# Optimization experiments

Measured on AMD Instinct MI355X. Metric: run time of the kernel, lower is better.

## Reference

```python
import jax, jax.numpy as jnp
import numpy as np

B, L, D, H = 2, 2048, 1024, 16
DK = D // H
DFF = 4 * D
EPS = 1e-5  # torch LayerNorm default


def setup_inputs() -> dict:
    key = jax.random.key(0)
    ks = jax.random.split(key, 12)
    w = lambda k, shp: (jax.random.normal(k, shp, jnp.float32) * 0.02)
    return {
        "x": jax.random.normal(ks[0], (B, L, D), jnp.float32),
        "y": jax.random.normal(ks[1], (B, L, D), jnp.float32),
        "Wq": w(ks[2], (D, D)), "bq": jnp.zeros((D,), jnp.float32),
        "Wk": w(ks[3], (D, D)), "bk": jnp.zeros((D,), jnp.float32),
        "Wv": w(ks[4], (D, D)), "bv": jnp.zeros((D,), jnp.float32),
        "Wo": w(ks[5], (D, D)), "bo": jnp.zeros((D,), jnp.float32),
        "W1": w(ks[6], (D, DFF)), "b1": jnp.zeros((DFF,), jnp.float32),
        "W2": w(ks[7], (DFF, D)), "b2": jnp.zeros((D,), jnp.float32),
        "ln1_w": jnp.ones((L, D), jnp.float32), "ln1_b": jnp.zeros((L, D), jnp.float32),
        "ln2_w": jnp.ones((L, D), jnp.float32), "ln2_b": jnp.zeros((L, D), jnp.float32),
    }


def _layernorm2d(t, w, b):
    # nn.LayerNorm(normalized_shape=[L, D]): normalize jointly over last two dims
    mu = jnp.mean(t, axis=(-2, -1), keepdims=True)
    var = jnp.mean((t - mu) ** 2, axis=(-2, -1), keepdims=True)
    return (t - mu) * jax.lax.rsqrt(var + EPS) * w + b


def _attention(q_in, kv_in, Wq, bq, Wk, bk, Wv, bv, Wo, bo):
    split = lambda t: t.reshape(B, L, H, DK).transpose(0, 2, 1, 3)  # [B,H,L,DK]
    q = split(q_in @ Wq + bq)
    k = split(kv_in @ Wk + bk)
    v = split(kv_in @ Wv + bv)
    scores = jnp.einsum("bhqd,bhkd->bhqk", q, k) / (DK ** 0.5)
    # NOTE: original applies torch.tril to SCORES (zeroes upper triangle,
    # NOT -inf), so future positions still contribute exp(0)=1 in softmax.
    scores = jnp.tril(scores)
    p_attn = jax.nn.softmax(scores, axis=-1)
    out = jnp.einsum("bhqk,bhkd->bhqd", p_attn, v)
    out = out.transpose(0, 2, 1, 3).reshape(B, L, D)
    return out @ Wo + bo


def reference(x, y, Wq, bq, Wk, bk, Wv, bv, Wo, bo, W1, b1, W2, b2,
              ln1_w, ln1_b, ln2_w, ln2_b):
    # sublayer 0: pre-norm y, attention(query=x, key=value=norm(y)), residual
    y1 = y + _attention(x, _layernorm2d(y, ln1_w, ln1_b),
                        Wq, bq, Wk, bk, Wv, bv, Wo, bo)
    # sublayer 1: pre-norm, FFN (dropout inactive in eval), residual
    h = jax.nn.relu(_layernorm2d(y1, ln2_w, ln2_b) @ W1 + b1)
    return y1 + h @ W2 + b2
```

## Files before the change

kernel.cpp:

```cpp
#include <hip/hip_runtime.h>
#include <math.h>

#define B 2
#define L 2048
#define D 1024
#define H 16
#define DK 64
#define DFF 4096
#define EPS 1e-5f

typedef short short8 __attribute__((ext_vector_type(8)));
typedef short short4v __attribute__((ext_vector_type(4)));
typedef float float4v __attribute__((ext_vector_type(4)));
typedef unsigned int u32;

__device__ inline short f2bf(float f) {
    unsigned u = __builtin_bit_cast(unsigned, f);
    u += 0x7fffu + ((u >> 16) & 1u);
    return (short)(u >> 16);
}

__device__ inline float bf2f(short s) {
    unsigned u = ((unsigned)(unsigned short)s) << 16;
    return __builtin_bit_cast(float, u);
}

#define GLOAD_LDS16(gp, lp)                                                  \
    __builtin_amdgcn_global_load_lds(                                        \
        (const __attribute__((address_space(1))) u32*)(const void*)(gp),     \
        (__attribute__((address_space(3))) u32*)(void*)(lp), 16, 0, 0)


__global__ __launch_bounds__(256) void red_partial(const float* __restrict__ X,
                                                   float* __restrict__ part) {
    int b = blockIdx.y;
    const float4* p = (const float4*)(X + (size_t)b * L * D);
    float s = 0.f, ss = 0.f;
    for (int idx = blockIdx.x * 256 + threadIdx.x; idx < L * D / 4; idx += 256 * 256) {
        float4 v = p[idx];
        s += v.x + v.y + v.z + v.w;
        ss += v.x * v.x + v.y * v.y + v.z * v.z + v.w * v.w;
    }
    __shared__ float sh0[256], sh1[256];
    sh0[threadIdx.x] = s; sh1[threadIdx.x] = ss;
    __syncthreads();
    for (int o = 128; o; o >>= 1) {
        if (threadIdx.x < o) {
            sh0[threadIdx.x] += sh0[threadIdx.x + o];
            sh1[threadIdx.x] += sh1[threadIdx.x + o];
        }
        __syncthreads();
    }
    if (threadIdx.x == 0) {
        part[(b * 256 + blockIdx.x) * 2 + 0] = sh0[0];
        part[(b * 256 + blockIdx.x) * 2 + 1] = sh1[0];
    }
}

__global__ __launch_bounds__(256) void red_final(const float* __restrict__ part,
                                                 float* __restrict__ stats) {
    int b = blockIdx.x;
    float s = part[(b * 256 + threadIdx.x) * 2 + 0];
    float ss = part[(b * 256 + threadIdx.x) * 2 + 1];
    __shared__ float sh0[256], sh1[256];
    sh0[threadIdx.x] = s; sh1[threadIdx.x] = ss;
    __syncthreads();
    for (int o = 128; o; o >>= 1) {
        if (threadIdx.x < o) {
            sh0[threadIdx.x] += sh0[threadIdx.x + o];
            sh1[threadIdx.x] += sh1[threadIdx.x + o];
        }
        __syncthreads();
    }
    if (threadIdx.x == 0) {
        const float invN = 1.f / (float)(L * D);
        float mu = sh0[0] * invN;
        float var = sh1[0] * invN - mu * mu;
        stats[b * 2 + 0] = mu;
        stats[b * 2 + 1] = rsqrtf(var + EPS);
    }
}

__global__ __launch_bounds__(256) void ln_apply_bf(const float* __restrict__ X,
                                                   const float* __restrict__ W,
                                                   const float* __restrict__ Bb,
                                                   const float* __restrict__ stats,
                                                   short* __restrict__ Yn) {
    int b = blockIdx.y;
    float mu = stats[b * 2 + 0];
    float rstd = stats[b * 2 + 1];
    size_t e = (size_t)(blockIdx.x * 256 + threadIdx.x) * 4;
    const float4 xv = *(const float4*)(X + (size_t)b * L * D + e);
    const float4 wv = *(const float4*)(W + e);
    const float4 bv = *(const float4*)(Bb + e);
    short4v o;
    o[0] = f2bf((xv.x - mu) * rstd * wv.x + bv.x);
    o[1] = f2bf((xv.y - mu) * rstd * wv.y + bv.y);
    o[2] = f2bf((xv.z - mu) * rstd * wv.z + bv.z);
    o[3] = f2bf((xv.w - mu) * rstd * wv.w + bv.w);
    *(short4v*)(Yn + (size_t)b * L * D + e) = o;
}

__global__ __launch_bounds__(256) void convert_bf(const float* __restrict__ X,
                                                  short* __restrict__ Y) {
    size_t e = (size_t)(blockIdx.x * 256 + threadIdx.x) * 4;
    const float4 v = *(const float4*)(X + e);
    short4v o = {f2bf(v.x), f2bf(v.y), f2bf(v.z), f2bf(v.w)};
    *(short4v*)(Y + e) = o;
}

__global__ __launch_bounds__(256) void wt_transpose(const float* __restrict__ W,
                                                    short* __restrict__ WT,
                                                    int K, int N) {
    __shared__ short tile[32][33];
    const int t = threadIdx.x;
    const int tx = t & 31, ty = t >> 5;
    const int k0 = blockIdx.y * 32, n0 = blockIdx.x * 32;
#pragma unroll
    for (int i = 0; i < 4; ++i) {
        const int k = ty + i * 8;
        tile[k][tx] = f2bf(W[(size_t)(k0 + k) * N + n0 + tx]);
    }
    __syncthreads();
#pragma unroll
    for (int i = 0; i < 4; ++i) {
        const int n = ty + i * 8;
        WT[(size_t)(n0 + n) * K + k0 + tx] = tile[tx][n];
    }
}


__global__ __launch_bounds__(256) void gemm_mfma(const short* __restrict__ A,
                                                 const short* __restrict__ BT,
                                                 const float* __restrict__ bias,
                                                 const float* __restrict__ Res,
                                                 void* __restrict__ Cout,
                                                 int M, int N, int K, int flags) {
    __shared__ short As[128 * 32];
    __shared__ short Bs[128 * 32];
    const int t = threadIdx.x;
    const int wave = t >> 6, lane = t & 63;
    const int m16 = lane & 15, q4 = lane >> 4;
    const int m0 = blockIdx.y * 128, n0 = blockIdx.x * 128;
    const int wm = (wave >> 1) * 64, wn = (wave & 1) * 64;

    float4v acc[4][4];
#pragma unroll
    for (int i = 0; i < 4; ++i)
#pragma unroll
        for (int j = 0; j < 4; ++j) acc[i][j] = (float4v){0.f, 0.f, 0.f, 0.f};

    for (int k0 = 0; k0 < K; k0 += 32) {
        __syncthreads();
#pragma unroll
        for (int pass = 0; pass < 2; ++pass) {
            const int idx = pass * 256 + t;
            const int row = idx >> 2;
            const int ko = (idx & 3) * 8;
            short* ldsA = &As[(pass * 256 + wave * 64) * 8];
            short* ldsB = &Bs[(pass * 256 + wave * 64) * 8];
            GLOAD_LDS16(A + (size_t)(m0 + row) * K + k0 + ko, ldsA);
            GLOAD_LDS16(BT + (size_t)(n0 + row) * K + k0 + ko, ldsB);
        }
        __syncthreads();

        short8 af[4], bf[4];
#pragma unroll
        for (int mi = 0; mi < 4; ++mi)
            af[mi] = *(const short8*)&As[(wm + mi * 16 + m16) * 32 + q4 * 8];
#pragma unroll
        for (int ni = 0; ni < 4; ++ni)
            bf[ni] = *(const short8*)&Bs[(wn + ni * 16 + m16) * 32 + q4 * 8];
#pragma unroll
        for (int mi = 0; mi < 4; ++mi)
#pragma unroll
            for (int ni = 0; ni < 4; ++ni)
                acc[mi][ni] = __builtin_amdgcn_mfma_f32_16x16x32_bf16(
                    af[mi], bf[ni], acc[mi][ni], 0, 0, 0);
    }

#pragma unroll
    for (int mi = 0; mi < 4; ++mi)
#pragma unroll
        for (int ni = 0; ni < 4; ++ni) {
            const int col = n0 + wn + ni * 16 + m16;
            const float bb = bias[col];
#pragma unroll
            for (int r = 0; r < 4; ++r) {
                const int row = m0 + wm + mi * 16 + q4 * 4 + r;
                float v = acc[mi][ni][r] + bb;
                if (Res) v += Res[(size_t)row * N + col];
                if (flags & 1) v = fmaxf(v, 0.f);
                if (flags & 2)
                    ((short*)Cout)[(size_t)row * N + col] = f2bf(v);
                else
                    ((float*)Cout)[(size_t)row * N + col] = v;
            }
        }
}


__global__ __launch_bounds__(256) void gemm_mfma_64(const short* __restrict__ A,
                                                    const short* __restrict__ BT,
                                                    const float* __restrict__ bias,
                                                    const float* __restrict__ Res,
                                                    void* __restrict__ Cout,
                                                    int M, int N, int K, int flags) {
    __shared__ short As[64 * 32];
    __shared__ short Bs[128 * 32];
    const int t = threadIdx.x;
    const int wave = t >> 6, lane = t & 63;
    const int m16 = lane & 15, q4 = lane >> 4;
    const int m0 = blockIdx.y * 64, n0 = blockIdx.x * 128;
    const int wm = (wave >> 1) * 32, wn = (wave & 1) * 64;

    float4v acc[2][4];
#pragma unroll
    for (int i = 0; i < 2; ++i)
#pragma unroll
        for (int j = 0; j < 4; ++j) acc[i][j] = (float4v){0.f, 0.f, 0.f, 0.f};

    for (int k0 = 0; k0 < K; k0 += 32) {
        __syncthreads();
        {
            const int row = t >> 2;
            const int ko = (t & 3) * 8;
            short* ldsA = &As[(wave * 64) * 8];
            GLOAD_LDS16(A + (size_t)(m0 + row) * K + k0 + ko, ldsA);
        }
#pragma unroll
        for (int pass = 0; pass < 2; ++pass) {
            const int idx = pass * 256 + t;
            const int row = idx >> 2;
            const int ko = (idx & 3) * 8;
            short* ldsB = &Bs[(pass * 256 + wave * 64) * 8];
            GLOAD_LDS16(BT + (size_t)(n0 + row) * K + k0 + ko, ldsB);
        }
        __syncthreads();

        short8 af[2], bf[4];
#pragma unroll
        for (int mi = 0; mi < 2; ++mi)
            af[mi] = *(const short8*)&As[(wm + mi * 16 + m16) * 32 + q4 * 8];
#pragma unroll
        for (int ni = 0; ni < 4; ++ni)
            bf[ni] = *(const short8*)&Bs[(wn + ni * 16 + m16) * 32 + q4 * 8];
#pragma unroll
        for (int mi = 0; mi < 2; ++mi)
#pragma unroll
            for (int ni = 0; ni < 4; ++ni)
                acc[mi][ni] = __builtin_amdgcn_mfma_f32_16x16x32_bf16(
                    af[mi], bf[ni], acc[mi][ni], 0, 0, 0);
    }

#pragma unroll
    for (int mi = 0; mi < 2; ++mi)
#pragma unroll
        for (int ni = 0; ni < 4; ++ni) {
            const int col = n0 + wn + ni * 16 + m16;
            const float bb = bias[col];
#pragma unroll
            for (int r = 0; r < 4; ++r) {
                const int row = m0 + wm + mi * 16 + q4 * 4 + r;
                float v = acc[mi][ni][r] + bb;
                if (Res) v += Res[(size_t)row * N + col];
                if (flags & 1) v = fmaxf(v, 0.f);
                if (flags & 2)
                    ((short*)Cout)[(size_t)row * N + col] = f2bf(v);
                else
                    ((float*)Cout)[(size_t)row * N + col] = v;
            }
        }
}


#define ASTR 72
#define SKV (2 * D)

__global__ __launch_bounds__(256) void v_tilesum(const short* __restrict__ KVg,
                                                 float* __restrict__ Vtile) {
    const int bh = blockIdx.x >> 5;
    const int kt = blockIdx.x & 31;
    const int b = bh >> 4, h = bh & (H - 1);
    const size_t baseV = (size_t)b * L * SKV + (size_t)h * DK + D;
    const int d = threadIdx.x & 63, g = threadIdx.x >> 6;
    float s = 0.f;
    for (int j = g * 16; j < g * 16 + 16; ++j)
        s += bf2f(KVg[baseV + (size_t)(kt * 64 + j) * SKV + d]);
    __shared__ float sh[4][64];
    sh[g][d] = s;
    __syncthreads();
    if (threadIdx.x < 64)
        Vtile[((size_t)bh * 32 + kt) * 64 + d] = sh[0][d] + sh[1][d] + sh[2][d] + sh[3][d];
}

__global__ __launch_bounds__(64) void v_suffix(const float* __restrict__ Vtile,
                                               float* __restrict__ Vsuf) {
    const int bh = blockIdx.x;
    const int d = threadIdx.x;
    float s = 0.f;
    Vsuf[((size_t)bh * 33 + 32) * 64 + d] = 0.f;
    for (int kt = 31; kt >= 0; --kt) {
        s += Vtile[((size_t)bh * 32 + kt) * 64 + d];
        Vsuf[((size_t)bh * 33 + kt) * 64 + d] = s;
    }
}


__device__ inline void attn_stage_load(const short* __restrict__ KVg,
                                       size_t baseK, int kt0, int sj, int sd8,
                                       short8* kr, short8* vr) {
#pragma unroll
    for (int rep = 0; rep < 2; ++rep) {
        const int j = rep * 32 + sj;
        const size_t g = baseK + (size_t)(kt0 + j) * SKV + sd8;
        kr[rep] = *(const short8*)(KVg + g);
        vr[rep] = *(const short8*)(KVg + g + D);
    }
}

__device__ inline void attn_stage_write(short* __restrict__ KbB,
                                        short* __restrict__ VtB,
                                        int sj, int sd8,
                                        const short8* kr, const short8* vr) {
    const int sm = sd8 >> 3;
#pragma unroll
    for (int rep = 0; rep < 2; ++rep) {
        const int j = rep * 32 + sj;
        *(short8*)&KbB[j * ASTR + sd8] = kr[rep];
        const int jsw = ((((j >> 3) ^ sm) << 3) | (j & 7));
#pragma unroll
        for (int i = 0; i < 8; ++i) VtB[(sd8 + i) * ASTR + jsw] = vr[rep][i];
    }
}

__global__ __launch_bounds__(256) void attn_mfma(const short* __restrict__ Qg,
                                                 const short* __restrict__ KVg,
                                                 const float* __restrict__ Vsuf,
                                                 short* __restrict__ O) {
    __shared__ alignas(16) short Kb[2][64 * ASTR];
    __shared__ alignas(16) short Vt[2][64 * ASTR];
    __shared__ alignas(16) short Pb[64 * ASTR];

    const int t = threadIdx.x;
    const int wave = t >> 6;
    const int lane = t & 63;
    const int m16 = lane & 15;
    const int q4 = lane >> 4;

    const int u = blockIdx.x & 15;
    const int bh = blockIdx.x >> 4;
    const int h = bh & (H - 1);
    const int b = bh >> 4;
    const size_t baseQ = (size_t)b * L * D + (size_t)h * DK;
    const size_t baseK = (size_t)b * L * SKV + (size_t)h * DK;

    const int sj = t >> 3;
    const int sd8 = (t & 7) * 8;

    const int irow = wave * 16 + m16;
    const int ig = irow >> 3;

#pragma unroll
    for (int pq = 0; pq < 2; ++pq) {
        const int qt = pq ? (31 - u) : u;
        const int q0 = qt * 64;
        const int rowA = q0 + wave * 16 + m16;

        short8 qf[2];
#pragma unroll
        for (int kc = 0; kc < 2; ++kc)
            qf[kc] = *(const short8*)(Qg + baseQ + (size_t)rowA * D + kc * 32 + q4 * 8);

        float lsum = 0.f;
        float4v acc[4];
#pragma unroll
        for (int f = 0; f < 4; ++f) acc[f] = (float4v){0.f, 0.f, 0.f, 0.f};

        {
            short8 kr[2], vr[2];
            attn_stage_load(KVg, baseK, 0, sj, sd8, kr, vr);
            attn_stage_write(&Kb[0][0], &Vt[0][0], sj, sd8, kr, vr);
        }
        __syncthreads();

        for (int kt = 0; kt <= qt; ++kt) {
            const int cur = kt & 1;
            const short* KbC = &Kb[cur][0];
            const short* VtC = &Vt[cur][0];

            short8 kr[2], vr[2];
            if (kt < qt)
                attn_stage_load(KVg, baseK, (kt + 1) * 64, sj, sd8, kr, vr);

            const bool diag = (kt == qt);

#pragma unroll
            for (int f = 0; f < 4; ++f) {
                const short8 kf0 = *(const short8*)&KbC[(f * 16 + m16) * ASTR + q4 * 8];
                const short8 kf1 = *(const short8*)&KbC[(f * 16 + m16) * ASTR + 32 + q4 * 8];
                float4v sv = {0.f, 0.f, 0.f, 0.f};
                sv = __builtin_amdgcn_mfma_f32_16x16x32_bf16(kf0, qf[0], sv, 0, 0, 0);
                sv = __builtin_amdgcn_mfma_f32_16x16x32_bf16(kf1, qf[1], sv, 0, 0, 0);

                float pv[4];
                if (diag) {
#pragma unroll
                    for (int r = 0; r < 4; ++r) {
                        const int jl = f * 16 + q4 * 4 + r;
                        pv[r] = (jl <= irow) ? __expf(sv[r] * 0.125f) : 1.0f;
                    }
                } else {
#pragma unroll
                    for (int r = 0; r < 4; ++r) pv[r] = __expf(sv[r] * 0.125f);
                }
                lsum += pv[0] + pv[1] + pv[2] + pv[3];

                short4v s4;
                s4[0] = f2bf(pv[0]); s4[1] = f2bf(pv[1]);
                s4[2] = f2bf(pv[2]); s4[3] = f2bf(pv[3]);
                const int jb = f * 2 + (q4 >> 1);
                *(short4v*)&Pb[irow * ASTR + (((jb ^ ig) << 3) | ((q4 & 1) << 2))] = s4;
            }

#pragma unroll
            for (int kc = 0; kc < 2; ++kc) {
                const short8 pf = *(const short8*)&Pb[irow * ASTR + (((kc * 4 + q4) ^ ig) << 3)];
#pragma unroll
                for (int f = 0; f < 4; ++f) {
                    const int d = f * 16 + m16;
                    const short8 vf = *(const short8*)&VtC[d * ASTR + (((kc * 4 + q4) ^ (d >> 3)) << 3)];
                    acc[f] = __builtin_amdgcn_mfma_f32_16x16x32_bf16(pf, vf, acc[f], 0, 0, 0);
                }
            }

            if (kt < qt)
                attn_stage_write(&Kb[cur ^ 1][0], &Vt[cur ^ 1][0], sj, sd8, kr, vr);
            __syncthreads();
        }

        float s = lsum;
        s += __shfl_xor(s, 16);
        s += __shfl_xor(s, 32);
        s += (float)(L - (qt + 1) * 64);
        const float inv = 1.0f / s;
        float invr[4];
#pragma unroll
        for (int r = 0; r < 4; ++r) invr[r] = __shfl(inv, q4 * 4 + r);

        const float* vs = Vsuf + ((size_t)bh * 33 + qt + 1) * 64;
#pragma unroll
        for (int f = 0; f < 4; ++f) {
            const float vadd = vs[f * 16 + m16];
#pragma unroll
            for (int r = 0; r < 4; ++r) {
                const int i = q0 + wave * 16 + q4 * 4 + r;
                O[baseQ + (size_t)i * D + f * 16 + m16] = f2bf((acc[f][r] + vadd) * invr[r]);
            }
        }
    }
}


extern "C" void kernel_launch(void* const* d_in, const int* in_sizes, int n_in,
                              void* d_out, int out_size, void* d_ws, size_t ws_size,
                              hipStream_t stream) {
    const float* x    = (const float*)d_in[0];
    const float* y    = (const float*)d_in[1];
    const float* Wq   = (const float*)d_in[2];
    const float* bq   = (const float*)d_in[3];
    const float* Wk   = (const float*)d_in[4];
    const float* bk   = (const float*)d_in[5];
    const float* Wv   = (const float*)d_in[6];
    const float* bv   = (const float*)d_in[7];
    const float* Wo   = (const float*)d_in[8];
    const float* bo   = (const float*)d_in[9];
    const float* W1   = (const float*)d_in[10];
    const float* b1   = (const float*)d_in[11];
    const float* W2   = (const float*)d_in[12];
    const float* b2   = (const float*)d_in[13];
    const float* ln1w = (const float*)d_in[14];
    const float* ln1b = (const float*)d_in[15];
    const float* ln2w = (const float*)d_in[16];
    const float* ln2b = (const float*)d_in[17];
    float* out = (float*)d_out;

    const size_t F = (size_t)B * L * D;
    char* p = (char*)d_ws;
    short* xb    = (short*)p; p += F * 2;
    short* ynb   = (short*)p; p += F * 2;
    short* qb    = (short*)p; p += F * 2;
    short* kvb   = (short*)p; p += 2 * F * 2;
    short* aob   = (short*)p; p += F * 2;
    short* y1nb  = (short*)p; p += F * 2;
    short* hb    = (short*)p; p += (size_t)B * L * DFF * 2;
    float* y1    = (float*)p; p += F * 4;
    short* WqT   = (short*)p; p += (size_t)D * D * 2;
    short* WkvT  = (short*)p; p += (size_t)D * 2 * D * 2;
    short* WoT   = (short*)p; p += (size_t)D * D * 2;
    short* W1T   = (short*)p; p += (size_t)D * DFF * 2;
    short* W2T   = (short*)p; p += (size_t)D * DFF * 2;
    float* biaskv= (float*)p; p += 2 * D * 4;
    float* vtile = (float*)p; p += (size_t)B * H * 32 * DK * 4;
    float* vsuf  = (float*)p; p += (size_t)B * H * 33 * DK * 4;
    float* part  = (float*)p; p += B * 256 * 2 * 4;
    float* stats = (float*)p;

    const int M = B * L;

    wt_transpose<<<dim3(D / 32, D / 32), 256, 0, stream>>>(Wq, WqT, D, D);
    wt_transpose<<<dim3(D / 32, D / 32), 256, 0, stream>>>(Wk, WkvT, D, D);
    wt_transpose<<<dim3(D / 32, D / 32), 256, 0, stream>>>(Wv, WkvT + (size_t)D * D, D, D);
    wt_transpose<<<dim3(D / 32, D / 32), 256, 0, stream>>>(Wo, WoT, D, D);
    wt_transpose<<<dim3(DFF / 32, D / 32), 256, 0, stream>>>(W1, W1T, D, DFF);
    wt_transpose<<<dim3(D / 32, DFF / 32), 256, 0, stream>>>(W2, W2T, DFF, D);
    hipMemcpyAsync(biaskv,     bk, D * sizeof(float), hipMemcpyDeviceToDevice, stream);
    hipMemcpyAsync(biaskv + D, bv, D * sizeof(float), hipMemcpyDeviceToDevice, stream);

    convert_bf<<<dim3(F / 1024), 256, 0, stream>>>(x, xb);

    red_partial<<<dim3(256, B), 256, 0, stream>>>(y, part);
    red_final<<<dim3(B), 256, 0, stream>>>(part, stats);
    ln_apply_bf<<<dim3(L * D / 1024, B), 256, 0, stream>>>(y, ln1w, ln1b, stats, ynb);

    gemm_mfma_64<<<dim3(D / 128, M / 64), 256, 0, stream>>>(xb, WqT, bq, nullptr, qb, M, D, D, 2);
    gemm_mfma<<<dim3(2 * D / 128, M / 128), 256, 0, stream>>>(ynb, WkvT, biaskv, nullptr, kvb, M, 2 * D, D, 2);

    v_tilesum<<<dim3(B * H * 32), 256, 0, stream>>>(kvb, vtile);
    v_suffix<<<dim3(B * H), 64, 0, stream>>>(vtile, vsuf);

    attn_mfma<<<dim3(B * H * 16), 256, 0, stream>>>(qb, kvb, vsuf, aob);

    gemm_mfma_64<<<dim3(D / 128, M / 64), 256, 0, stream>>>(aob, WoT, bo, y, y1, M, D, D, 0);

    red_partial<<<dim3(256, B), 256, 0, stream>>>(y1, part);
    red_final<<<dim3(B), 256, 0, stream>>>(part, stats);
    ln_apply_bf<<<dim3(L * D / 1024, B), 256, 0, stream>>>(y1, ln2w, ln2b, stats, y1nb);

    gemm_mfma<<<dim3(DFF / 128, M / 128), 256, 0, stream>>>(y1nb, W1T, b1, nullptr, hb, M, DFF, D, 3);

    gemm_mfma_64<<<dim3(D / 128, M / 64), 256, 0, stream>>>(hb, W2T, b2, y1, out, M, D, DFF, 0);
}
```

Measured before the change: 484.5 us.

## Double-buffer GEMM LDS tiles with K=64 steps and XOR-swizzled layout

Replaces the single-buffered GEMM kernels with versions that keep two LDS buffers, so the next K-tile is loaded while MFMAs run on the current one. The K step grows from 32 to 64, which halves the number of barriers per tile. An XOR swizzle on the 16-byte column slots is meant to avoid LDS bank conflicts on the fragment reads. LDS use per block rises, which may lower occupancy. The W1 GEMM still uses the old gemm_mfma kernel.

```diff
diff --git a/kernel.cpp b/kernel.cpp
--- a/kernel.cpp
+++ b/kernel.cpp
@@ -200,19 +200,20 @@
 }
 
 
-__global__ __launch_bounds__(256) void gemm_mfma_64(const short* __restrict__ A,
-                                                    const short* __restrict__ BT,
-                                                    const float* __restrict__ bias,
-                                                    const float* __restrict__ Res,
-                                                    void* __restrict__ Cout,
-                                                    int M, int N, int K, int flags) {
-    __shared__ short As[64 * 32];
-    __shared__ short Bs[128 * 32];
+__global__ __launch_bounds__(256) void gemm_db64(const short* __restrict__ A,
+                                                 const short* __restrict__ BT,
+                                                 const float* __restrict__ bias,
+                                                 const float* __restrict__ Res,
+                                                 void* __restrict__ Cout,
+                                                 int M, int N, int K, int flags) {
+    __shared__ short As[2][64 * 64];
+    __shared__ short Bs[2][128 * 64];
     const int t = threadIdx.x;
     const int wave = t >> 6, lane = t & 63;
     const int m16 = lane & 15, q4 = lane >> 4;
     const int m0 = blockIdx.y * 64, n0 = blockIdx.x * 128;
     const int wm = (wave >> 1) * 32, wn = (wave & 1) * 64;
+    const int xorm = m16 & 7;
 
     float4v acc[2][4];
 #pragma unroll
@@ -220,41 +221,141 @@
 #pragma unroll
         for (int j = 0; j < 4; ++j) acc[i][j] = (float4v){0.f, 0.f, 0.f, 0.f};
 
-    for (int k0 = 0; k0 < K; k0 += 32) {
+    auto stage = [&](int buf, int k0) {
+#pragma unroll
+        for (int p = 0; p < 2; ++p) {
+            const int s = p * 256 + t;
+            const int row = s >> 3;
+            const int col = ((s & 7) ^ (row & 7)) * 8;
+            short* lds = &As[buf][(p * 256 + wave * 64) * 8];
+            GLOAD_LDS16(A + (size_t)(m0 + row) * K + k0 + col, lds);
+        }
+#pragma unroll
+        for (int p = 0; p < 4; ++p) {
+            const int s = p * 256 + t;
+            const int row = s >> 3;
+            const int col = ((s & 7) ^ (row & 7)) * 8;
+            short* lds = &Bs[buf][(p * 256 + wave * 64) * 8];
+            GLOAD_LDS16(BT + (size_t)(n0 + row) * K + k0 + col, lds);
+        }
+    };
+
+    auto compute = [&](int buf) {
+#pragma unroll
+        for (int kk = 0; kk < 2; ++kk) {
+            const int slot = ((kk * 4 + q4) ^ xorm) * 8;
+            short8 af[2], bf[4];
+#pragma unroll
+            for (int mi = 0; mi < 2; ++mi)
+                af[mi] = *(const short8*)&As[buf][(wm + mi * 16 + m16) * 64 + slot];
+#pragma unroll
+            for (int ni = 0; ni < 4; ++ni)
+                bf[ni] = *(const short8*)&Bs[buf][(wn + ni * 16 + m16) * 64 + slot];
+#pragma unroll
+            for (int mi = 0; mi < 2; ++mi)
+#pragma unroll
+                for (int ni = 0; ni < 4; ++ni)
+                    acc[mi][ni] = __builtin_amdgcn_mfma_f32_16x16x32_bf16(
+                        af[mi], bf[ni], acc[mi][ni], 0, 0, 0);
+        }
+    };
+
+    stage(0, 0);
+    __syncthreads();
+    const int nt = K >> 6;
+    for (int ti = 0; ti < nt; ++ti) {
+        const int cur = ti & 1;
+        if (ti + 1 < nt) stage(cur ^ 1, (ti + 1) * 64);
+        compute(cur);
         __syncthreads();
-        {
-            const int row = t >> 2;
-            const int ko = (t & 3) * 8;
-            short* ldsA = &As[(wave * 64) * 8];
-            GLOAD_LDS16(A + (size_t)(m0 + row) * K + k0 + ko, ldsA);
-        }
-#pragma unroll
-        for (int pass = 0; pass < 2; ++pass) {
-            const int idx = pass * 256 + t;
-            const int row = idx >> 2;
-            const int ko = (idx & 3) * 8;
-            short* ldsB = &Bs[(pass * 256 + wave * 64) * 8];
-            GLOAD_LDS16(BT + (size_t)(n0 + row) * K + k0 + ko, ldsB);
-        }
+    }
+
+#pragma unroll
+    for (int mi = 0; mi < 2; ++mi)
+#pragma unroll
+        for (int ni = 0; ni < 4; ++ni) {
+            const int col = n0 + wn + ni * 16 + m16;
+            const float bb = bias[col];
+#pragma unroll
+            for (int r = 0; r < 4; ++r) {
+                const int row = m0 + wm + mi * 16 + q4 * 4 + r;
+                float v = acc[mi][ni][r] + bb;
+                if (Res) v += Res[(size_t)row * N + col];
+                if (flags & 1) v = fmaxf(v, 0.f);
+                if (flags & 2)
+                    ((short*)Cout)[(size_t)row * N + col] = f2bf(v);
+                else
+                    ((float*)Cout)[(size_t)row * N + col] = v;
+            }
+        }
+}
+
+__global__ __launch_bounds__(256) void gemm_db128(const short* __restrict__ A,
+                                                  const short* __restrict__ BT,
+                                                  const float* __restrict__ bias,
+                                                  const float* __restrict__ Res,
+                                                  void* __restrict__ Cout,
+                                                  int M, int N, int K, int flags) {
+    __shared__ short As[2][128 * 64];
+    __shared__ short Bs[2][128 * 64];
+    const int t = threadIdx.x;
+    const int wave = t >> 6, lane = t & 63;
+    const int m16 = lane & 15, q4 = lane >> 4;
+    const int m0 = blockIdx.y * 128, n0 = blockIdx.x * 128;
+    const int wm = (wave >> 1) * 64, wn = (wave & 1) * 64;
+    const int xorm = m16 & 7;
+
+    float4v acc[4][4];
+#pragma unroll
+    for (int i = 0; i < 4; ++i)
+#pragma unroll
+        for (int j = 0; j < 4; ++j) acc[i][j] = (float4v){0.f, 0.f, 0.f, 0.f};
+
+    auto stage = [&](int buf, int k0) {
+#pragma unroll
+        for (int p = 0; p < 4; ++p) {
+            const int s = p * 256 + t;
+            const int row = s >> 3;
+            const int col = ((s & 7) ^ (row & 7)) * 8;
+            short* ldsA = &As[buf][(p * 256 + wave * 64) * 8];
+            short* ldsB = &Bs[buf][(p * 256 + wave * 64) * 8];
+            GLOAD_LDS16(A + (size_t)(m0 + row) * K + k0 + col, ldsA);
+            GLOAD_LDS16(BT + (size_t)(n0 + row) * K + k0 + col, ldsB);
+        }
+    };
+
+    auto compute = [&](int buf) {
+#pragma unroll
+        for (int kk = 0; kk < 2; ++kk) {
+            const int slot = ((kk * 4 + q4) ^ xorm) * 8;
+            short8 af[4], bf[4];
+#pragma unroll
+            for (int mi = 0; mi < 4; ++mi)
+                af[mi] = *(const short8*)&As[buf][(wm + mi * 16 + m16) * 64 + slot];
+#pragma unroll
+            for (int ni = 0; ni < 4; ++ni)
+                bf[ni] = *(const short8*)&Bs[buf][(wn + ni * 16 + m16) * 64 + slot];
+#pragma unroll
+            for (int mi = 0; mi < 4; ++mi)
+#pragma unroll
+                for (int ni = 0; ni < 4; ++ni)
+                    acc[mi][ni] = __builtin_amdgcn_mfma_f32_16x16x32_bf16(
+                        af[mi], bf[ni], acc[mi][ni], 0, 0, 0);
+        }
+    };
+
+    stage(0, 0);
+    __syncthreads();
+    const int nt = K >> 6;
+    for (int ti = 0; ti < nt; ++ti) {
+        const int cur = ti & 1;
+        if (ti + 1 < nt) stage(cur ^ 1, (ti + 1) * 64);
+        compute(cur);
         __syncthreads();
-
-        short8 af[2], bf[4];
-#pragma unroll
-        for (int mi = 0; mi < 2; ++mi)
-            af[mi] = *(const short8*)&As[(wm + mi * 16 + m16) * 32 + q4 * 8];
-#pragma unroll
-        for (int ni = 0; ni < 4; ++ni)
-            bf[ni] = *(const short8*)&Bs[(wn + ni * 16 + m16) * 32 + q4 * 8];
-#pragma unroll
-        for (int mi = 0; mi < 2; ++mi)
-#pragma unroll
-            for (int ni = 0; ni < 4; ++ni)
-                acc[mi][ni] = __builtin_amdgcn_mfma_f32_16x16x32_bf16(
-                    af[mi], bf[ni], acc[mi][ni], 0, 0, 0);
-    }
-
-#pragma unroll
-    for (int mi = 0; mi < 2; ++mi)
+    }
+
+#pragma unroll
+    for (int mi = 0; mi < 4; ++mi)
 #pragma unroll
         for (int ni = 0; ni < 4; ++ni) {
             const int col = n0 + wn + ni * 16 + m16;
@@ -523,15 +624,15 @@
     red_final<<<dim3(B), 256, 0, stream>>>(part, stats);
     ln_apply_bf<<<dim3(L * D / 1024, B), 256, 0, stream>>>(y, ln1w, ln1b, stats, ynb);
 
-    gemm_mfma_64<<<dim3(D / 128, M / 64), 256, 0, stream>>>(xb, WqT, bq, nullptr, qb, M, D, D, 2);
-    gemm_mfma<<<dim3(2 * D / 128, M / 128), 256, 0, stream>>>(ynb, WkvT, biaskv, nullptr, kvb, M, 2 * D, D, 2);
+    gemm_db64<<<dim3(D / 128, M / 64), 256, 0, stream>>>(xb, WqT, bq, nullptr, qb, M, D, D, 2);
+    gemm_db128<<<dim3(2 * D / 128, M / 128), 256, 0, stream>>>(ynb, WkvT, biaskv, nullptr, kvb, M, 2 * D, D, 2);
 
     v_tilesum<<<dim3(B * H * 32), 256, 0, stream>>>(kvb, vtile);
     v_suffix<<<dim3(B * H), 64, 0, stream>>>(vtile, vsuf);
 
     attn_mfma<<<dim3(B * H * 16), 256, 0, stream>>>(qb, kvb, vsuf, aob);
 
-    gemm_mfma_64<<<dim3(D / 128, M / 64), 256, 0, stream>>>(aob, WoT, bo, y, y1, M, D, D, 0);
+    gemm_db64<<<dim3(D / 128, M / 64), 256, 0, stream>>>(aob, WoT, bo, y, y1, M, D, D, 0);
 
     red_partial<<<dim3(256, B), 256, 0, stream>>>(y1, part);
     red_final<<<dim3(B), 256, 0, stream>>>(part, stats);
@@ -539,5 +640,5 @@
 
     gemm_mfma<<<dim3(DFF / 128, M / 128), 256, 0, stream>>>(y1nb, W1T, b1, nullptr, hb, M, DFF, D, 3);
 
-    gemm_mfma_64<<<dim3(D / 128, M / 64), 256, 0, stream>>>(hb, W2T, b2, y1, out, M, D, DFF, 0);
-}
+    gemm_db64<<<dim3(D / 128, M / 64), 256, 0, stream>>>(hb, W2T, b2, y1, out, M, D, DFF, 0);
+}
```

Result: faster. 459.8 us (-5.1%).

## Triple-buffer GEMM LDS tiles with async prefetch and XOR swizzle

Applied to the files above, without the earlier changes.

Both GEMM kernels now use a three-stage LDS ring fed by direct global-to-LDS loads. Each iteration waits only on older loads through vmcnt and takes one barrier instead of two, so the prefetch of tile k+2 overlaps the MFMA work on tile k. The LDS columns are XOR-swizzled to cut bank conflicts on the fragment reads, and the 64-row kernel moves to a K-tile of 64. The cost is more shared memory per block, which may lower occupancy, plus a redundant trailing load of the last tile that keeps the vmcnt accounting simple.

```diff
diff --git a/kernel.cpp b/kernel.cpp
--- a/kernel.cpp
+++ b/kernel.cpp
@@ -130,57 +130,83 @@
 }
 
 
-__global__ __launch_bounds__(256) void gemm_mfma(const short* __restrict__ A,
-                                                 const short* __restrict__ BT,
-                                                 const float* __restrict__ bias,
-                                                 const float* __restrict__ Res,
-                                                 void* __restrict__ Cout,
-                                                 int M, int N, int K, int flags) {
-    __shared__ short As[128 * 32];
-    __shared__ short Bs[128 * 32];
+__global__ __launch_bounds__(256) void gemm_p3_64(const short* __restrict__ A,
+                                                  const short* __restrict__ BT,
+                                                  const float* __restrict__ bias,
+                                                  const float* __restrict__ Res,
+                                                  void* __restrict__ Cout,
+                                                  int M, int N, int K, int flags) {
+    __shared__ short As[3][64 * 64];
+    __shared__ short Bs[3][128 * 64];
     const int t = threadIdx.x;
     const int wave = t >> 6, lane = t & 63;
     const int m16 = lane & 15, q4 = lane >> 4;
-    const int m0 = blockIdx.y * 128, n0 = blockIdx.x * 128;
-    const int wm = (wave >> 1) * 64, wn = (wave & 1) * 64;
-
-    float4v acc[4][4];
-#pragma unroll
-    for (int i = 0; i < 4; ++i)
+    const int m0 = blockIdx.y * 64, n0 = blockIdx.x * 128;
+    const int wm = (wave >> 1) * 32, wn = (wave & 1) * 64;
+    const int xorm = m16 & 7;
+
+    float4v acc[2][4];
+#pragma unroll
+    for (int i = 0; i < 2; ++i)
 #pragma unroll
         for (int j = 0; j < 4; ++j) acc[i][j] = (float4v){0.f, 0.f, 0.f, 0.f};
 
-    for (int k0 = 0; k0 < K; k0 += 32) {
-        __syncthreads();
-#pragma unroll
-        for (int pass = 0; pass < 2; ++pass) {
-            const int idx = pass * 256 + t;
-            const int row = idx >> 2;
-            const int ko = (idx & 3) * 8;
-            short* ldsA = &As[(pass * 256 + wave * 64) * 8];
-            short* ldsB = &Bs[(pass * 256 + wave * 64) * 8];
-            GLOAD_LDS16(A + (size_t)(m0 + row) * K + k0 + ko, ldsA);
-            GLOAD_LDS16(BT + (size_t)(n0 + row) * K + k0 + ko, ldsB);
-        }
-        __syncthreads();
-
-        short8 af[4], bf[4];
-#pragma unroll
-        for (int mi = 0; mi < 4; ++mi)
-            af[mi] = *(const short8*)&As[(wm + mi * 16 + m16) * 32 + q4 * 8];
-#pragma unroll
-        for (int ni = 0; ni < 4; ++ni)
-            bf[ni] = *(const short8*)&Bs[(wn + ni * 16 + m16) * 32 + q4 * 8];
-#pragma unroll
-        for (int mi = 0; mi < 4; ++mi)
+    auto stage = [&](int buf, int k0) {
+#pragma unroll
+        for (int p = 0; p < 2; ++p) {
+            const int s = p * 256 + t;
+            const int row = s >> 3;
+            const int col = ((s & 7) ^ (row & 7)) * 8;
+            short* lds = &As[buf][(p * 256 + wave * 64) * 8];
+            GLOAD_LDS16(A + (size_t)(m0 + row) * K + k0 + col, lds);
+        }
+#pragma unroll
+        for (int p = 0; p < 4; ++p) {
+            const int s = p * 256 + t;
+            const int row = s >> 3;
+            const int col = ((s & 7) ^ (row & 7)) * 8;
+            short* lds = &Bs[buf][(p * 256 + wave * 64) * 8];
+            GLOAD_LDS16(BT + (size_t)(n0 + row) * K + k0 + col, lds);
+        }
+    };
+
+    auto compute = [&](int buf) {
+#pragma unroll
+        for (int kk = 0; kk < 2; ++kk) {
+            const int slot = ((kk * 4 + q4) ^ xorm) * 8;
+            short8 af[2], bf[4];
+#pragma unroll
+            for (int mi = 0; mi < 2; ++mi)
+                af[mi] = *(const short8*)&As[buf][(wm + mi * 16 + m16) * 64 + slot];
 #pragma unroll
             for (int ni = 0; ni < 4; ++ni)
-                acc[mi][ni] = __builtin_amdgcn_mfma_f32_16x16x32_bf16(
-                    af[mi], bf[ni], acc[mi][ni], 0, 0, 0);
-    }
-
-#pragma unroll
-    for (int mi = 0; mi < 4; ++mi)
+                bf[ni] = *(const short8*)&Bs[buf][(wn + ni * 16 + m16) * 64 + slot];
+#pragma unroll
+            for (int mi = 0; mi < 2; ++mi)
+#pragma unroll
+                for (int ni = 0; ni < 4; ++ni)
+                    acc[mi][ni] = __builtin_amdgcn_mfma_f32_16x16x32_bf16(
+                        af[mi], bf[ni], acc[mi][ni], 0, 0, 0);
+        }
+    };
+
+    const int nt = K >> 6;
+    stage(0, 0);
+    stage(1, 64);
+    int s0 = 0, s2 = 2;
+    for (int ti = 0; ti < nt; ++ti) {
+        asm volatile("s_waitcnt vmcnt(6)" ::: "memory");
+        __builtin_amdgcn_s_barrier();
+        __builtin_amdgcn_sched_barrier(0);
+        const int kn = (ti + 2 < nt ? ti + 2 : nt - 1) << 6;
+        stage(s2, kn);
+        compute(s0);
+        s0 = (s0 == 2) ? 0 : s0 + 1;
+        s2 = (s2 == 2) ? 0 : s2 + 1;
+    }
+
+#pragma unroll
+    for (int mi = 0; mi < 2; ++mi)
 #pragma unroll
         for (int ni = 0; ni < 4; ++ni) {
             const int col = n0 + wn + ni * 16 + m16;
@@ -199,62 +225,74 @@
         }
 }
 
-
-__global__ __launch_bounds__(256) void gemm_mfma_64(const short* __restrict__ A,
-                                                    const short* __restrict__ BT,
-                                                    const float* __restrict__ bias,
-                                                    const float* __restrict__ Res,
-                                                    void* __restrict__ Cout,
-                                                    int M, int N, int K, int flags) {
-    __shared__ short As[64 * 32];
-    __shared__ short Bs[128 * 32];
+__global__ __launch_bounds__(256) void gemm_p3_128(const short* __restrict__ A,
+                                                   const short* __restrict__ BT,
+                                                   const float* __restrict__ bias,
+                                                   const float* __restrict__ Res,
+                                                   void* __restrict__ Cout,
+                                                   int M, int N, int K, int flags) {
+    __shared__ short As[3][128 * 32];
+    __shared__ short Bs[3][128 * 32];
     const int t = threadIdx.x;
     const int wave = t >> 6, lane = t & 63;
     const int m16 = lane & 15, q4 = lane >> 4;
-    const int m0 = blockIdx.y * 64, n0 = blockIdx.x * 128;
-    const int wm = (wave >> 1) * 32, wn = (wave & 1) * 64;
-
-    float4v acc[2][4];
-#pragma unroll
-    for (int i = 0; i < 2; ++i)
+    const int m0 = blockIdx.y * 128, n0 = blockIdx.x * 128;
+    const int wm = (wave >> 1) * 64, wn = (wave & 1) * 64;
+    const int xorm = m16 & 3;
+
+    float4v acc[4][4];
+#pragma unroll
+    for (int i = 0; i < 4; ++i)
 #pragma unroll
         for (int j = 0; j < 4; ++j) acc[i][j] = (float4v){0.f, 0.f, 0.f, 0.f};
 
-    for (int k0 = 0; k0 < K; k0 += 32) {
-        __syncthreads();
-        {
-            const int row = t >> 2;
-            const int ko = (t & 3) * 8;
-            short* ldsA = &As[(wave * 64) * 8];
-            GLOAD_LDS16(A + (size_t)(m0 + row) * K + k0 + ko, ldsA);
-        }
-#pragma unroll
-        for (int pass = 0; pass < 2; ++pass) {
-            const int idx = pass * 256 + t;
-            const int row = idx >> 2;
-            const int ko = (idx & 3) * 8;
-            short* ldsB = &Bs[(pass * 256 + wave * 64) * 8];
-            GLOAD_LDS16(BT + (size_t)(n0 + row) * K + k0 + ko, ldsB);
-        }
-        __syncthreads();
-
-        short8 af[2], bf[4];
-#pragma unroll
-        for (int mi = 0; mi < 2; ++mi)
-            af[mi] = *(const short8*)&As[(wm + mi * 16 + m16) * 32 + q4 * 8];
+    auto stage = [&](int buf, int k0) {
+#pragma unroll
+        for (int p = 0; p < 2; ++p) {
+            const int s = p * 256 + t;
+            const int row = s >> 2;
+            const int col = ((s & 3) ^ (row & 3)) * 8;
+            short* ldsA = &As[buf][(p * 256 + wave * 64) * 8];
+            short* ldsB = &Bs[buf][(p * 256 + wave * 64) * 8];
+            GLOAD_LDS16(A + (size_t)(m0 + row) * K + k0 + col, ldsA);
+            GLOAD_LDS16(BT + (size_t)(n0 + row) * K + k0 + col, ldsB);
+        }
+    };
+
+    auto compute = [&](int buf) {
+        const int slot = (q4 ^ xorm) * 8;
+        short8 af[4], bf[4];
+#pragma unroll
+        for (int mi = 0; mi < 4; ++mi)
+            af[mi] = *(const short8*)&As[buf][(wm + mi * 16 + m16) * 32 + slot];
 #pragma unroll
         for (int ni = 0; ni < 4; ++ni)
-            bf[ni] = *(const short8*)&Bs[(wn + ni * 16 + m16) * 32 + q4 * 8];
-#pragma unroll
-        for (int mi = 0; mi < 2; ++mi)
+            bf[ni] = *(const short8*)&Bs[buf][(wn + ni * 16 + m16) * 32 + slot];
+#pragma unroll
+        for (int mi = 0; mi < 4; ++mi)
 #pragma unroll
             for (int ni = 0; ni < 4; ++ni)
                 acc[mi][ni] = __builtin_amdgcn_mfma_f32_16x16x32_bf16(
                     af[mi], bf[ni], acc[mi][ni], 0, 0, 0);
-    }
-
-#pragma unroll
-    for (int mi = 0; mi < 2; ++mi)
+    };
+
+    const int nt = K >> 5;
+    stage(0, 0);
+    stage(1, 32);
+    int s0 = 0, s2 = 2;
+    for (int ti = 0; ti < nt; ++ti) {
+        asm volatile("s_waitcnt vmcnt(4)" ::: "memory");
+        __builtin_amdgcn_s_barrier();
+        __builtin_amdgcn_sched_barrier(0);
+        const int kn = (ti + 2 < nt ? ti + 2 : nt - 1) << 5;
+        stage(s2, kn);
+        compute(s0);
+        s0 = (s0 == 2) ? 0 : s0 + 1;
+        s2 = (s2 == 2) ? 0 : s2 + 1;
+    }
+
+#pragma unroll
+    for (int mi = 0; mi < 4; ++mi)
 #pragma unroll
         for (int ni = 0; ni < 4; ++ni) {
             const int col = n0 + wn + ni * 16 + m16;
@@ -523,21 +561,21 @@
     red_final<<<dim3(B), 256, 0, stream>>>(part, stats);
     ln_apply_bf<<<dim3(L * D / 1024, B), 256, 0, stream>>>(y, ln1w, ln1b, stats, ynb);
 
-    gemm_mfma_64<<<dim3(D / 128, M / 64), 256, 0, stream>>>(xb, WqT, bq, nullptr, qb, M, D, D, 2);
-    gemm_mfma<<<dim3(2 * D / 128, M / 128), 256, 0, stream>>>(ynb, WkvT, biaskv, nullptr, kvb, M, 2 * D, D, 2);
+    gemm_p3_64<<<dim3(D / 128, M / 64), 256, 0, stream>>>(xb, WqT, bq, nullptr, qb, M, D, D, 2);
+    gemm_p3_128<<<dim3(2 * D / 128, M / 128), 256, 0, stream>>>(ynb, WkvT, biaskv, nullptr, kvb, M, 2 * D, D, 2);
 
     v_tilesum<<<dim3(B * H * 32), 256, 0, stream>>>(kvb, vtile);
     v_suffix<<<dim3(B * H), 64, 0, stream>>>(vtile, vsuf);
 
     attn_mfma<<<dim3(B * H * 16), 256, 0, stream>>>(qb, kvb, vsuf, aob);
 
-    gemm_mfma_64<<<dim3(D / 128, M / 64), 256, 0, stream>>>(aob, WoT, bo, y, y1, M, D, D, 0);
+    gemm_p3_64<<<dim3(D / 128, M / 64), 256, 0, stream>>>(aob, WoT, bo, y, y1, M, D, D, 0);
 
     red_partial<<<dim3(256, B), 256, 0, stream>>>(y1, part);
     red_final<<<dim3(B), 256, 0, stream>>>(part, stats);
     ln_apply_bf<<<dim3(L * D / 1024, B), 256, 0, stream>>>(y1, ln2w, ln2b, stats, y1nb);
 
-    gemm_mfma<<<dim3(DFF / 128, M / 128), 256, 0, stream>>>(y1nb, W1T, b1, nullptr, hb, M, DFF, D, 3);
-
-    gemm_mfma_64<<<dim3(D / 128, M / 64), 256, 0, stream>>>(hb, W2T, b2, y1, out, M, D, DFF, 0);
-}
+    gemm_p3_128<<<dim3(DFF / 128, M / 128), 256, 0, stream>>>(y1nb, W1T, b1, nullptr, hb, M, DFF, D, 3);
+
+    gemm_p3_64<<<dim3(D / 128, M / 64), 256, 0, stream>>>(hb, W2T, b2, y1, out, M, D, DFF, 0);
+}
```

After: 457.2 us. -5.6%, faster.
